# Performance work log

Measured on AMD Instinct MI355X. Metric: run time of the kernel, lower is better.

Reference implementation:

```python
import jax, jax.numpy as jnp
import numpy as np

# ---- static config (mirrors Net.__init__) ----
N_NODES, N_EDGES = 4000, 20000
N_PROTS, D = 919, 512            # node_emb: Embedding(919, 512); F_in = D (divide_input=False)
TOWERS, F_OUT = 4, D // 4        # F_out = out_channels // towers = 128
EDGE_D = 50
N_GRAPHS, N_CLASSES = 32, 10
N_LAYERS = 2
EPS_BN, EPS_STD = 1e-5, 1e-5

# deg histogram passed to PNAConv; only avg_deg['log'] matters for the scalers used
DEG_HIST = np.array([0., 800., 1200., 900., 600., 300., 150., 50.])
AVG_DEG_LOG = float((np.log(np.arange(DEG_HIST.size) + 1.0) * DEG_HIST).sum() / DEG_HIST.sum())


def setup_inputs() -> dict:
    key = jax.random.key(0)
    ks = jax.random.split(key, 16)
    g = lambda i, shape, s=0.05: (jax.random.normal(ks[i], shape, jnp.float32) * s)
    return dict(
        node_emb_w=g(0, (N_PROTS, D), 0.1),
        edge_emb_w=g(1, (2, EDGE_D), 0.1),
        pe_w=g(2, (2, D)), pe_b=jnp.zeros((D,), jnp.float32),
        edge_enc_w=g(3, (N_LAYERS, EDGE_D, D)), edge_enc_b=jnp.zeros((N_LAYERS, D), jnp.float32),
        pre_w=g(4, (N_LAYERS, TOWERS, 3 * D, D)), pre_b=jnp.zeros((N_LAYERS, TOWERS, D), jnp.float32),
        post_w=g(5, (N_LAYERS, TOWERS, 13 * D, F_OUT)), post_b=jnp.zeros((N_LAYERS, TOWERS, F_OUT), jnp.float32),
        lin_w=g(6, (N_LAYERS, D, D)), lin_b=jnp.zeros((N_LAYERS, D), jnp.float32),
        bn_gamma=jnp.ones((N_LAYERS, D), jnp.float32), bn_beta=jnp.zeros((N_LAYERS, D), jnp.float32),
        acts=jax.random.normal(ks[7], (N_NODES, 2), jnp.float32),
        fc1_w=g(8, (D, 2 * D)), fc1_b=jnp.zeros((2 * D,), jnp.float32),
        fc_out_w=g(9, (2 * D, N_CLASSES)), fc_out_b=jnp.zeros((N_CLASSES,), jnp.float32),
        prelu_a=jnp.float32(0.25),
        global_idx=jax.random.randint(ks[10], (N_NODES,), 0, N_PROTS),
        sign=jax.random.randint(ks[11], (N_EDGES,), 0, 2),
        edge_index=jax.random.randint(ks[12], (2, N_EDGES), 0, N_NODES),
        batch=jnp.sort(jax.random.randint(ks[13], (N_NODES,), 0, N_GRAPHS)),
    )


def _pna_layer(x, src, dst, e, pre_w, pre_b, post_w, post_b, lin_w, lin_b):
    # x: [N, D], e: [E, D] (edge_encoder output), pre_w: [T, 3D, D], post_w: [T, 13D, F_OUT]
    N, E = x.shape[0], src.shape[0]
    # pre-NN on cat([x_i, x_j, edge_attr]) expressed as split matmuls (pre_layers=1 -> single Linear)
    Wi, Wj, We = pre_w[:, :D], pre_w[:, D:2 * D], pre_w[:, 2 * D:]
    m = (jnp.einsum('ef,tfd->etd', x[dst], Wi)
         + jnp.einsum('ef,tfd->etd', x[src], Wj)
         + jnp.einsum('ef,tfd->etd', e, We) + pre_b)          # [E, T, D]
    # multi-aggregation at destination nodes: mean / min / max / std
    cnt = jax.ops.segment_sum(jnp.ones((E,), m.dtype), dst, N)  # in-degree
    has = (cnt > 0)[:, None, None]
    deg = jnp.maximum(cnt, 1.0)[:, None, None]                  # clamp(1) as in PyG
    s1 = jax.ops.segment_sum(m, dst, N)
    s2 = jax.ops.segment_sum(m * m, dst, N)
    mean = s1 / deg
    std = jnp.sqrt(jax.nn.relu(s2 / deg - mean * mean) + EPS_STD)
    mn = jnp.where(has, jax.ops.segment_min(m, dst, N), 0.0)
    mx = jnp.where(has, jax.ops.segment_max(m, dst, N), 0.0)
    agg = jnp.concatenate([mean, mn, mx, std], axis=-1)         # [N, T, 4D]
    # degree scalers: identity, amplification, attenuation
    amp = jnp.log(deg + 1.0) / AVG_DEG_LOG
    out = jnp.concatenate([agg, agg * amp, agg / amp], axis=-1)  # [N, T, 12D]
    # post-NN on cat([x, out]) as split matmuls (post_layers=1)
    Wx, Wo = post_w[:, :D], post_w[:, D:]
    o = (jnp.einsum('nf,tfd->ntd', x, Wx)
         + jnp.einsum('ntf,tfd->ntd', out, Wo) + post_b)        # [N, T, F_OUT]
    return o.reshape(N, TOWERS * F_OUT) @ lin_w + lin_b         # [N, D]


def reference(node_emb_w, edge_emb_w, pe_w, pe_b, edge_enc_w, edge_enc_b,
              pre_w, pre_b, post_w, post_b, lin_w, lin_b, bn_gamma, bn_beta,
              acts, fc1_w, fc1_b, fc_out_w, fc_out_b, prelu_a,
              global_idx, sign, edge_index, batch):
    src, dst = edge_index[0], edge_index[1]
    x = node_emb_w[global_idx] + (acts @ pe_w + pe_b)           # node_emb + PostEncoding
    ea = edge_emb_w[sign]                                       # [E, 50]
    for l in range(N_LAYERS):
        e = ea @ edge_enc_w[l] + edge_enc_b[l]                  # shared edge encoder
        h = _pna_layer(x, src, dst, e, pre_w[l], pre_b[l], post_w[l], post_b[l], lin_w[l], lin_b[l])
        mu = h.mean(axis=0)
        var = ((h - mu) ** 2).mean(axis=0)                      # training-mode BatchNorm (biased var)
        x = jax.nn.relu(bn_gamma[l] * (h - mu) * jax.lax.rsqrt(var + EPS_BN) + bn_beta[l])
    pooled = jax.ops.segment_sum(x, batch, N_GRAPHS)            # global_add_pool
    z = pooled @ fc1_w + fc1_b
    z = jnp.where(z > 0, z, prelu_a * z)                        # PReLU
    logits = z @ fc_out_w + fc_out_b
    return jax.nn.log_softmax(logits, axis=-1)
```

## Files before the change

### kernel.cpp

```cpp
#include <hip/hip_runtime.h>
#include <hip/hip_bf16.h>
#include <float.h>

#define NN 4000
#define NE 20000
#define DD 512
#define NT 4
#define FO 128
#define NG 32
#define NC 10
#define XGW 4096
#define AVGLOG 1.2548916493836102f
#define EPS_STD_ 1e-5f
#define EPS_BN_ 1e-5f

typedef __bf16 bf16x8 __attribute__((ext_vector_type(8)));
typedef float  f32x4  __attribute__((ext_vector_type(4)));

__device__ __forceinline__ void async_copy16(const void* g, void* l) {
    __builtin_amdgcn_global_load_lds((const __attribute__((address_space(1))) void*)g,
                                     (__attribute__((address_space(3))) void*)l, 16, 0, 0);
}

__global__ __launch_bounds__(256) void k_xg(const __bf16* __restrict__ XB, const __bf16* __restrict__ WCAT,
                                            const float* __restrict__ pb,
                                            __bf16* __restrict__ XG, float* __restrict__ OF,
                                            float* __restrict__ BN, float* __restrict__ PL, int zero_pl) {
    const int m0 = blockIdx.y * 128, n0 = blockIdx.x * 128;
    __shared__ __bf16 As[2 * 128 * 32];
    __shared__ __bf16 Bs[2 * 128 * 32];
    const int tid = threadIdx.x;
    const int wave = tid >> 6, lane = tid & 63;
    const int wm = (wave >> 1) * 64, wn = (wave & 1) * 64;
    const int fr = lane & 15, fq = lane >> 4;
    const int fk = fq * 8;
    const int srow = lane >> 2, skc = (lane & 3) * 8;

    f32x4 acc[4][4];
    const f32x4 zero = {0.f, 0.f, 0.f, 0.f};
#pragma unroll
    for (int i = 0; i < 4; ++i)
#pragma unroll
        for (int j = 0; j < 4; ++j) acc[i][j] = zero;

    for (int k0 = 0; k0 < 512; k0 += 64) {
#pragma unroll
        for (int p = 0; p < 2; ++p) {
#pragma unroll
            for (int q = 0; q < 2; ++q) {
                const int row = wave * 32 + q * 16 + srow;
                int ar = m0 + row; if (ar > NN - 1) ar = NN - 1;
                async_copy16(XB + (size_t)ar * 512 + k0 + p * 32 + skc,
                             As + p * 4096 + wave * 1024 + q * 512);
                async_copy16(WCAT + (size_t)(n0 + row) * 512 + k0 + p * 32 + skc,
                             Bs + p * 4096 + wave * 1024 + q * 512);
            }
        }
        __syncthreads();
#pragma unroll
        for (int p = 0; p < 2; ++p) {
            bf16x8 af[4], bfr[4];
#pragma unroll
            for (int mi = 0; mi < 4; ++mi) af[mi]  = *(const bf16x8*)(As + p * 4096 + (wm + mi * 16 + fr) * 32 + fk);
#pragma unroll
            for (int ni = 0; ni < 4; ++ni) bfr[ni] = *(const bf16x8*)(Bs + p * 4096 + (wn + ni * 16 + fr) * 32 + fk);
#pragma unroll
            for (int mi = 0; mi < 4; ++mi)
#pragma unroll
                for (int ni = 0; ni < 4; ++ni)
                    acc[mi][ni] = __builtin_amdgcn_mfma_f32_16x16x32_bf16(af[mi], bfr[ni], acc[mi][ni], 0, 0, 0);
        }
        __syncthreads();
    }
    if (n0 < 4096) {
#pragma unroll
        for (int mi = 0; mi < 4; ++mi) {
#pragma unroll
            for (int ni = 0; ni < 4; ++ni) {
                const int col = n0 + wn + ni * 16 + fr;
                const int rb = m0 + wm + mi * 16 + fq * 4;
#pragma unroll
                for (int r = 0; r < 4; ++r) {
                    const int rowc = rb + r;
                    if (rowc < NN) XG[(size_t)rowc * XGW + col] = (__bf16)acc[mi][ni][r];
                }
            }
        }
    } else {
        const int ocb = n0 - 4096;
#pragma unroll
        for (int mi = 0; mi < 4; ++mi) {
#pragma unroll
            for (int ni = 0; ni < 4; ++ni) {
                const int oc = ocb + wn + ni * 16 + fr;
                const float bv = pb[oc];
                const int rb = m0 + wm + mi * 16 + fq * 4;
#pragma unroll
                for (int r = 0; r < 4; ++r) {
                    const int rowc = rb + r;
                    if (rowc < NN) OF[(size_t)rowc * 512 + oc] = acc[mi][ni][r] + bv;
                }
            }
        }
    }
    if (blockIdx.x == 32 && blockIdx.y == 0) {
        BN[tid] = 0.f; BN[256 + tid] = 0.f; BN[512 + tid] = 0.f; BN[768 + tid] = 0.f;
        if (zero_pl)
            for (int i = tid; i < NG * DD; i += 256) PL[i] = 0.f;
    }
}

__global__ __launch_bounds__(256) void k_gw(const __bf16* __restrict__ AB, const __bf16* __restrict__ WTT,
                                            const float* __restrict__ amp, const float* __restrict__ ramp,
                                            __bf16* __restrict__ GWPb) {
    const int t = blockIdx.z & 3, kh = blockIdx.z >> 2;
    const int xg = blockIdx.x;
    const int m0 = blockIdx.y * 128;
    const __bf16* A  = AB  + (size_t)t * 2048 + (size_t)kh * 1024;
    const __bf16* BT = WTT + (size_t)t * 384 * 2048 + (size_t)xg * 128 * 2048 + (size_t)kh * 1024;
    __shared__ __bf16 As[2 * 128 * 32];
    __shared__ __bf16 Bs[2 * 128 * 32];
    const int tid = threadIdx.x;
    const int wave = tid >> 6, lane = tid & 63;
    const int wm = (wave >> 1) * 64, wn = (wave & 1) * 64;
    const int fr = lane & 15, fq = lane >> 4;
    const int fk = fq * 8;
    const int srow = lane >> 2, skc = (lane & 3) * 8;

    f32x4 acc[4][4];
    const f32x4 zero = {0.f, 0.f, 0.f, 0.f};
#pragma unroll
    for (int i = 0; i < 4; ++i)
#pragma unroll
        for (int j = 0; j < 4; ++j) acc[i][j] = zero;

    for (int k0 = 0; k0 < 1024; k0 += 64) {
#pragma unroll
        for (int p = 0; p < 2; ++p) {
#pragma unroll
            for (int q = 0; q < 2; ++q) {
                const int row = wave * 32 + q * 16 + srow;
                int ar = m0 + row; if (ar > NN - 1) ar = NN - 1;
                async_copy16(A + (size_t)ar * 8192 + k0 + p * 32 + skc,
                             As + p * 4096 + wave * 1024 + q * 512);
                async_copy16(BT + (size_t)row * 2048 + k0 + p * 32 + skc,
                             Bs + p * 4096 + wave * 1024 + q * 512);
            }
        }
        __syncthreads();
#pragma unroll
        for (int p = 0; p < 2; ++p) {
            bf16x8 af[4], bfr[4];
#pragma unroll
            for (int mi = 0; mi < 4; ++mi) af[mi]  = *(const bf16x8*)(As + p * 4096 + (wm + mi * 16 + fr) * 32 + fk);
#pragma unroll
            for (int ni = 0; ni < 4; ++ni) bfr[ni] = *(const bf16x8*)(Bs + p * 4096 + (wn + ni * 16 + fr) * 32 + fk);
#pragma unroll
            for (int mi = 0; mi < 4; ++mi)
#pragma unroll
                for (int ni = 0; ni < 4; ++ni)
                    acc[mi][ni] = __builtin_amdgcn_mfma_f32_16x16x32_bf16(af[mi], bfr[ni], acc[mi][ni], 0, 0, 0);
        }
        __syncthreads();
    }
    const int p = xg * 2 + kh;
    __bf16* P = GWPb + (size_t)p * NN * 512 + (size_t)t * 128;
#pragma unroll
    for (int mi = 0; mi < 4; ++mi) {
        const int rb = m0 + wm + mi * 16 + fq * 4;
#pragma unroll
        for (int r = 0; r < 4; ++r) {
            const int row = rb + r;
            if (row < NN) {
                const float w = (xg == 0) ? 1.0f : (xg == 1 ? amp[row] : ramp[row]);
#pragma unroll
                for (int ni = 0; ni < 4; ++ni)
                    P[(size_t)row * 512 + wn + ni * 16 + fr] = (__bf16)(acc[mi][ni][r] * w);
            }
        }
    }
}

__global__ void k_combine(const float* __restrict__ OF, const __bf16* __restrict__ GWPb,
                          __bf16* __restrict__ OB) {
    const size_t idx8 = ((size_t)blockIdx.x * 256 + threadIdx.x) * 8;
    float4 o0 = *(const float4*)(OF + idx8);
    float4 o1 = *(const float4*)(OF + idx8 + 4);
    float s[8] = {o0.x, o0.y, o0.z, o0.w, o1.x, o1.y, o1.z, o1.w};
#pragma unroll
    for (int p = 0; p < 6; ++p) {
        bf16x8 g = *(const bf16x8*)(GWPb + (size_t)p * NN * 512 + idx8);
#pragma unroll
        for (int i = 0; i < 8; ++i) s[i] += (float)g[i];
    }
    bf16x8 ov;
#pragma unroll
    for (int i = 0; i < 8; ++i) ov[i] = (__bf16)s[i];
    *(bf16x8*)(OB + idx8) = ov;
}

__global__ __launch_bounds__(256) void k_lin(const __bf16* __restrict__ OB, const __bf16* __restrict__ WLINT,
                                             const float* __restrict__ bl, float* __restrict__ H,
                                             float* __restrict__ BN) {
    const int n0c = blockIdx.x * 128, m0 = blockIdx.y * 64;
    __shared__ __bf16 As[64 * 32];
    __shared__ __bf16 Bs[128 * 32];
    __shared__ float bnS[128], bnQ[128];
    const int tid = threadIdx.x;
    if (tid < 128) { bnS[tid] = 0.f; bnQ[tid] = 0.f; }
    const int wave = tid >> 6, lane = tid & 63;
    const int wr = wave >> 1, wc = wave & 1;
    const int fr = lane & 15, fq = lane >> 4;
    f32x4 acc[2][4];
    const f32x4 zero = {0.f, 0.f, 0.f, 0.f};
#pragma unroll
    for (int i = 0; i < 2; ++i)
#pragma unroll
        for (int j = 0; j < 4; ++j) acc[i][j] = zero;

    const int ar = tid >> 2, akc = (tid & 3) * 8;
    int arow = m0 + ar; if (arow > NN - 1) arow = NN - 1;
    for (int k0 = 0; k0 < 512; k0 += 32) {
        async_copy16(OB + (size_t)arow * 512 + k0 + akc, As + tid * 8);
#pragma unroll
        for (int i = 0; i < 2; ++i) {
            const int cb = tid + 256 * i;
            const int br = cb >> 2, bkc = (cb & 3) * 8;
            async_copy16(WLINT + (size_t)(n0c + br) * 512 + k0 + bkc, Bs + cb * 8);
        }
        __syncthreads();
        bf16x8 a[2], b[4];
#pragma unroll
        for (int mi = 0; mi < 2; ++mi) a[mi] = *(const bf16x8*)(As + (wr * 32 + mi * 16 + fr) * 32 + fq * 8);
#pragma unroll
        for (int ni = 0; ni < 4; ++ni) b[ni] = *(const bf16x8*)(Bs + (wc * 64 + ni * 16 + fr) * 32 + fq * 8);
#pragma unroll
        for (int mi = 0; mi < 2; ++mi)
#pragma unroll
            for (int ni = 0; ni < 4; ++ni)
                acc[mi][ni] = __builtin_amdgcn_mfma_f32_16x16x32_bf16(a[mi], b[ni], acc[mi][ni], 0, 0, 0);
        __syncthreads();
    }
#pragma unroll
    for (int ni = 0; ni < 4; ++ni) {
        const int lc = wc * 64 + ni * 16 + fr;
        const int col = n0c + lc;
        const float bv = bl[col];
        float s = 0.f, q = 0.f;
#pragma unroll
        for (int mi = 0; mi < 2; ++mi) {
#pragma unroll
            for (int r = 0; r < 4; ++r) {
                const int rowc = m0 + wr * 32 + mi * 16 + fq * 4 + r;
                if (rowc < NN) {
                    const float v = acc[mi][ni][r] + bv;
                    H[(size_t)rowc * 512 + col] = v;
                    s += v; q += v * v;
                }
            }
        }
        atomicAdd(&bnS[lc], s); atomicAdd(&bnQ[lc], q);
    }
    __syncthreads();
    if (tid < 128) {
        atomicAdd(&BN[n0c + tid], bnS[tid]);
        atomicAdd(&BN[512 + n0c + tid], bnQ[tid]);
    }
}

__device__ __forceinline__ void tr32(const float* __restrict__ S, int sld,
                                     __bf16* __restrict__ D, int dld, int tx, int ty) {
    __shared__ float t[32][33];
    const int y0 = ty * 4;
#pragma unroll
    for (int i = 0; i < 4; ++i) t[y0 + i][tx] = S[(size_t)(y0 + i) * sld + tx];
    __syncthreads();
#pragma unroll
    for (int i = 0; i < 4; ++i) D[(size_t)(y0 + i) * dld + tx] = (__bf16)t[tx][y0 + i];
}

__global__ __launch_bounds__(256) void k_tr(const float* __restrict__ pre_w, const float* __restrict__ post_w,
                                            const float* __restrict__ lin_w,
                                            const float* __restrict__ eemb, const float* __restrict__ eew_b,
                                            const float* __restrict__ eeb_b, const float* __restrict__ pre_b,
                                            __bf16* __restrict__ WCAT, __bf16* __restrict__ WTT,
                                            __bf16* __restrict__ WLINT, float* __restrict__ EM) {
    int id = blockIdx.x;
    const int lay = (id >= 5696) ? 1 : 0;
    id -= lay * 5696;
    const float* pw   = pre_w  + (size_t)lay * NT * 3 * 512 * 512;
    const float* pow_ = post_w + (size_t)lay * NT * 6656 * 128;
    const float* lw   = lin_w  + (size_t)lay * 512 * 512;
    const float* eew  = eew_b  + (size_t)lay * 50 * 512;
    const float* eeb  = eeb_b  + (size_t)lay * 512;
    const float* pb   = pre_b  + (size_t)lay * NT * 512;
    __bf16* WCATl  = WCAT  + (size_t)lay * 4608 * 512;
    __bf16* WTTl   = WTT   + (size_t)lay * NT * 384 * 2048;
    __bf16* WLINTl = WLINT + (size_t)lay * 512 * 512;
    float*  EMl    = EM    + (size_t)lay * 4096;
    const int tx = threadIdx.x & 31, ty = threadIdx.x >> 5;
    if (id < 2048) {
        const int z = id >> 8, r = id & 255;
        const int t = z & 3, half = z >> 2;
        const int x = r & 15, y = r >> 4;
        const float* S = pw + ((size_t)(t * 1536 + half * 512 + y * 32)) * 512 + x * 32;
        __bf16* D = WCATl + ((size_t)(half * 2048 + t * 512 + x * 32)) * 512 + y * 32;
        tr32(S, 512, D, 512, tx, ty);
    } else if (id < 2304) {
        const int id3 = id - 2048;
        const int t = id3 >> 6, r = id3 & 63;
        const int x = r & 3, y = r >> 2;
        const float* S = pow_ + ((size_t)(t * 6656 + y * 32)) * 128 + x * 32;
        __bf16* D = WCATl + ((size_t)(4096 + t * 128 + x * 32)) * 512 + y * 32;
        tr32(S, 128, D, 512, tx, ty);
    } else if (id < 5376) {
        const int id4 = id - 2304;
        const int z = id4 >> 8, r = id4 & 255;
        const int t = z / 3, w = z % 3;
        const int x = r & 3, y = r >> 2;
        const float* S = pow_ + ((size_t)(t * 6656 + 512 + w * 2048 + y * 32)) * 128 + x * 32;
        __bf16* D = WTTl + (size_t)t * 384 * 2048 + ((size_t)(w * 128 + x * 32)) * 2048 + y * 32;
        tr32(S, 128, D, 2048, tx, ty);
    } else if (id < 5632) {
        const int r = id - 5376;
        const int x = r & 15, y = r >> 4;
        const float* S = lw + (size_t)y * 32 * 512 + x * 32;
        __bf16* D = WLINTl + (size_t)x * 32 * 512 + y * 32;
        tr32(S, 512, D, 512, tx, ty);
    } else {
        __shared__ float eks[512];
        __shared__ float part[4][64];
        const int tid = threadIdx.x;
        const int id5 = id - 5632;
        const int k = id5 >> 5;
        const int g0 = (id5 & 31) * 64;
#pragma unroll
        for (int h = 0; h < 2; ++h) {
            const int f = tid + h * 256;
            float s = eeb[f];
            for (int c = 0; c < 50; ++c) s += eemb[k * 50 + c] * eew[(size_t)c * 512 + f];
            eks[f] = s;
        }
        __syncthreads();
        const int wave = tid >> 6, lane = tid & 63;
        const int g = g0 + lane;
        const int t = g >> 9, d = g & 511;
        const float* Wp = pw + ((size_t)(t * 1536 + 1024)) * 512 + d;
        float s = 0.f;
        const int f0 = wave * 128;
#pragma unroll 4
        for (int f = f0; f < f0 + 128; ++f) s += eks[f] * Wp[(size_t)f * 512];
        part[wave][lane] = s;
        __syncthreads();
        if (tid < 64) {
            const int gg = g0 + tid;
            EMl[k * 2048 + gg] = pb[gg] + part[0][tid] + part[1][tid] + part[2][tid] + part[3][tid];
        }
    }
}

__global__ void k_count(const int* __restrict__ dst, int* __restrict__ cnt) {
    int e = blockIdx.x * 256 + threadIdx.x;
    if (e < NE) atomicAdd(&cnt[dst[e]], 1);
}

__global__ __launch_bounds__(1024) void k_scan_bx(const int* __restrict__ cnt, int* __restrict__ offs,
                                                  float* __restrict__ amp, float* __restrict__ ramp,
                                                  const float* __restrict__ nemb, const float* __restrict__ acts,
                                                  const float* __restrict__ pew, const float* __restrict__ peb,
                                                  const int* __restrict__ gidx, __bf16* __restrict__ XB) {
    const int t = threadIdx.x;
    if (blockIdx.x == 0) {
        __shared__ int part[1024];
        const int base = t * 4;
        int loc[4]; int s = 0;
#pragma unroll
        for (int i = 0; i < 4; ++i) { int v = (base + i < NN) ? cnt[base + i] : 0; loc[i] = s; s += v; }
        part[t] = s;
        __syncthreads();
        for (int o = 1; o < 1024; o <<= 1) {
            int v = (t >= o) ? part[t - o] : 0;
            __syncthreads();
            part[t] += v;
            __syncthreads();
        }
        const int pre = (t > 0) ? part[t - 1] : 0;
#pragma unroll
        for (int i = 0; i < 4; ++i) if (base + i < NN) offs[base + i] = pre + loc[i];
        if (t == 1023) offs[NN] = part[1023];
        for (int n = t; n < NN; n += 1024) {
            float deg = fmaxf((float)cnt[n], 1.0f);
            float a = logf(deg + 1.0f) / AVGLOG;
            amp[n] = a; ramp[n] = 1.0f / a;
        }
    } else {
        const int idx = (blockIdx.x - 1) * 1024 + t;
        const int n = idx >> 9, d = idx & 511;
        float v = nemb[(size_t)gidx[n] * DD + d] + acts[n * 2] * pew[d] + acts[n * 2 + 1] * pew[DD + d] + peb[d];
        XB[idx] = (__bf16)v;
    }
}

__global__ void k_fill(const int* __restrict__ src, const int* __restrict__ dst,
                       const int* __restrict__ sgn, const int* __restrict__ offs,
                       int* __restrict__ fill, int* __restrict__ epack) {
    int e = blockIdx.x * 256 + threadIdx.x;
    if (e < NE) {
        int d = dst[e];
        int pos = offs[d] + atomicAdd(&fill[d], 1);
        epack[pos] = (src[e] << 1) | sgn[e];
    }
}

__global__ __launch_bounds__(256) void k_agg(const __bf16* __restrict__ XG, const float* __restrict__ EM,
                                             const int* __restrict__ offs, const int* __restrict__ cnt,
                                             const int* __restrict__ epack, __bf16* __restrict__ AB) {
    const int n = blockIdx.x;
    const int g = threadIdx.x * 8;
    __shared__ int se[64];
    const int j0 = offs[n];
    const int deg = offs[n + 1] - j0;
    const int degc = deg < 64 ? deg : 64;
    if (threadIdx.x < degc) se[threadIdx.x] = epack[j0 + threadIdx.x];
    __syncthreads();
    float xid[8], em0[8], em1[8];
    {
        bf16x8 xb = *(const bf16x8*)(XG + (size_t)n * XGW + g);
#pragma unroll
        for (int i = 0; i < 8; ++i) xid[i] = (float)xb[i];
    }
    *(float4*)&em0[0] = *(const float4*)&EM[g];
    *(float4*)&em0[4] = *(const float4*)&EM[g + 4];
    *(float4*)&em1[0] = *(const float4*)&EM[2048 + g];
    *(float4*)&em1[4] = *(const float4*)&EM[2048 + g + 4];
    float s1[8], s2[8], mn[8], mx[8];
#pragma unroll
    for (int i = 0; i < 8; ++i) { s1[i] = 0.f; s2[i] = 0.f; mn[i] = FLT_MAX; mx[i] = -FLT_MAX; }

    int jj = 0;
    for (; jj + 2 <= degc; jj += 2) {
        const int e0 = se[jj], e1 = se[jj + 1];
        bf16x8 x0 = *(const bf16x8*)(XG + (size_t)(e0 >> 1) * XGW + 2048 + g);
        bf16x8 x1 = *(const bf16x8*)(XG + (size_t)(e1 >> 1) * XGW + 2048 + g);
        const int sg0 = e0 & 1, sg1 = e1 & 1;
#pragma unroll
        for (int i = 0; i < 8; ++i) {
            float m = xid[i] + (float)x0[i] + (sg0 ? em1[i] : em0[i]);
            s1[i] += m; s2[i] += m * m;
            mn[i] = fminf(mn[i], m); mx[i] = fmaxf(mx[i], m);
        }
#pragma unroll
        for (int i = 0; i < 8; ++i) {
            float m = xid[i] + (float)x1[i] + (sg1 ? em1[i] : em0[i]);
            s1[i] += m; s2[i] += m * m;
            mn[i] = fminf(mn[i], m); mx[i] = fmaxf(mx[i], m);
        }
    }
    if (jj < degc) {
        const int e0 = se[jj];
        bf16x8 x0 = *(const bf16x8*)(XG + (size_t)(e0 >> 1) * XGW + 2048 + g);
        const int sg0 = e0 & 1;
#pragma unroll
        for (int i = 0; i < 8; ++i) {
            float m = xid[i] + (float)x0[i] + (sg0 ? em1[i] : em0[i]);
            s1[i] += m; s2[i] += m * m;
            mn[i] = fminf(mn[i], m); mx[i] = fmaxf(mx[i], m);
        }
    }
    for (int j = 64; j < deg; ++j) {
        const int e0 = epack[j0 + j];
        bf16x8 x0 = *(const bf16x8*)(XG + (size_t)(e0 >> 1) * XGW + 2048 + g);
        const int sg0 = e0 & 1;
#pragma unroll
        for (int i = 0; i < 8; ++i) {
            float m = xid[i] + (float)x0[i] + (sg0 ? em1[i] : em0[i]);
            s1[i] += m; s2[i] += m * m;
            mn[i] = fminf(mn[i], m); mx[i] = fmaxf(mx[i], m);
        }
    }
    const int c = deg;
    const float degf = fmaxf((float)c, 1.0f);
    const float rdeg = 1.0f / degf;
    bf16x8 vmean, vmn, vmx, vsd;
#pragma unroll
    for (int i = 0; i < 8; ++i) {
        float mean = s1[i] * rdeg;
        float var = s2[i] * rdeg - mean * mean;
        float sd = sqrtf(fmaxf(var, 0.f) + EPS_STD_);
        float mnv = (c == 0) ? 0.f : mn[i];
        float mxv = (c == 0) ? 0.f : mx[i];
        vmean[i] = (__bf16)mean; vmn[i] = (__bf16)mnv; vmx[i] = (__bf16)mxv; vsd[i] = (__bf16)sd;
    }
    const int t = g >> 9, d = g & 511;
    __bf16* base = AB + (size_t)n * 8192 + (size_t)t * 2048 + d;
    *(bf16x8*)(base + 0 * DD) = vmean;
    *(bf16x8*)(base + 1 * DD) = vmn;
    *(bf16x8*)(base + 2 * DD) = vmx;
    *(bf16x8*)(base + 3 * DD) = vsd;
}

__global__ void k_bnapply(const float* __restrict__ H, const float* __restrict__ BN,
                          const float* __restrict__ gamma, const float* __restrict__ beta,
                          __bf16* __restrict__ XB, float* __restrict__ PL,
                          const int* __restrict__ batch, int last) {
    int idx = blockIdx.x * 256 + threadIdx.x;
    int n = idx >> 9, d = idx & 511;
    float mu = BN[d] * (1.0f / NN);
    float var = BN[512 + d] * (1.0f / NN) - mu * mu;
    float v = gamma[d] * (H[idx] - mu) * rsqrtf(var + EPS_BN_) + beta[d];
    v = fmaxf(v, 0.f);
    if (last) atomicAdd(&PL[(size_t)batch[n] * DD + d], v);
    else XB[idx] = (__bf16)v;
}

__global__ __launch_bounds__(128) void k_fc1(const float* __restrict__ PL, const float* __restrict__ W1,
                                             const float* __restrict__ b1, const float* __restrict__ pa,
                                             float* __restrict__ Z) {
    const int g = blockIdx.x >> 3;
    const int j = (blockIdx.x & 7) * 128 + threadIdx.x;
    __shared__ float pl[512];
    for (int i = threadIdx.x; i < 512; i += 128) pl[i] = PL[(size_t)g * 512 + i];
    __syncthreads();
    const float* w = W1 + j;
    float s0 = 0.f, s1 = 0.f, s2 = 0.f, s3 = 0.f;
#pragma unroll 2
    for (int f = 0; f < 512; f += 4) {
        s0 += pl[f + 0] * w[(size_t)(f + 0) * 1024];
        s1 += pl[f + 1] * w[(size_t)(f + 1) * 1024];
        s2 += pl[f + 2] * w[(size_t)(f + 2) * 1024];
        s3 += pl[f + 3] * w[(size_t)(f + 3) * 1024];
    }
    float s = b1[j] + ((s0 + s1) + (s2 + s3));
    const float a = *pa;
    Z[(size_t)g * 1024 + j] = s > 0.f ? s : a * s;
}

__global__ __launch_bounds__(64) void k_out(const float* __restrict__ Z, const float* __restrict__ Wo,
                                            const float* __restrict__ bo, float* __restrict__ out) {
    const int g = blockIdx.x, t = threadIdx.x;
    float part[NC];
#pragma unroll
    for (int c = 0; c < NC; ++c) part[c] = 0.f;
    for (int f = t; f < 1024; f += 64) {
        const float zv = Z[(size_t)g * 1024 + f];
#pragma unroll
        for (int c = 0; c < NC; ++c) part[c] += zv * Wo[(size_t)f * NC + c];
    }
#pragma unroll
    for (int off = 32; off > 0; off >>= 1)
#pragma unroll
        for (int c = 0; c < NC; ++c) part[c] += __shfl_down(part[c], off);
    if (t == 0) {
        float lg[NC], mxv = -FLT_MAX;
#pragma unroll
        for (int c = 0; c < NC; ++c) { lg[c] = part[c] + bo[c]; mxv = fmaxf(mxv, lg[c]); }
        float se = 0.f;
#pragma unroll
        for (int c = 0; c < NC; ++c) se += expf(lg[c] - mxv);
        const float lse = mxv + logf(se);
#pragma unroll
        for (int c = 0; c < NC; ++c) out[g * NC + c] = lg[c] - lse;
    }
}

extern "C" void kernel_launch(void* const* d_in, const int* in_sizes, int n_in,
                              void* d_out, int out_size, void* d_ws, size_t ws_size,
                              hipStream_t stream) {
    const float* node_emb_w = (const float*)d_in[0];
    const float* edge_emb_w = (const float*)d_in[1];
    const float* pe_w   = (const float*)d_in[2];
    const float* pe_b   = (const float*)d_in[3];
    const float* edge_enc_w = (const float*)d_in[4];
    const float* edge_enc_b = (const float*)d_in[5];
    const float* pre_w  = (const float*)d_in[6];
    const float* pre_b  = (const float*)d_in[7];
    const float* post_w = (const float*)d_in[8];
    const float* post_b = (const float*)d_in[9];
    const float* lin_w  = (const float*)d_in[10];
    const float* lin_b  = (const float*)d_in[11];
    const float* bn_gamma = (const float*)d_in[12];
    const float* bn_beta  = (const float*)d_in[13];
    const float* acts   = (const float*)d_in[14];
    const float* fc1_w  = (const float*)d_in[15];
    const float* fc1_b  = (const float*)d_in[16];
    const float* fc_out_w = (const float*)d_in[17];
    const float* fc_out_b = (const float*)d_in[18];
    const float* prelu_a  = (const float*)d_in[19];
    const int* global_idx = (const int*)d_in[20];
    const int* sgn        = (const int*)d_in[21];
    const int* edge_index = (const int*)d_in[22];
    const int* batch      = (const int*)d_in[23];
    float* out = (float*)d_out;

    char* W = (char*)d_ws;
    size_t off = 0;
    auto alloc = [&](size_t bytes) { void* p = W + off; off += (bytes + 63) & ~(size_t)63; return p; };
    __bf16* XB    = (__bf16*)alloc((size_t)NN * DD * 2);
    float*  H     = (float*)alloc((size_t)NN * DD * 4);
    __bf16* XG    = (__bf16*)alloc((size_t)NN * XGW * 2);
    __bf16* AB    = (__bf16*)alloc((size_t)NN * 8192 * 2);
    float*  OF    = (float*)alloc((size_t)NN * DD * 4);
    __bf16* GWPb  = (__bf16*)alloc((size_t)6 * NN * 512 * 2);
    __bf16* OB    = (__bf16*)alloc((size_t)NN * DD * 2);
    __bf16* WCAT  = (__bf16*)alloc((size_t)2 * 4608 * 512 * 2);
    __bf16* WTT   = (__bf16*)alloc((size_t)2 * NT * 384 * 2048 * 2);
    __bf16* WLINT = (__bf16*)alloc((size_t)2 * 512 * 512 * 2);
    float*  EM    = (float*)alloc((size_t)2 * 2 * 2048 * 4);
    float*  BN    = (float*)alloc(1024 * 4);
    float*  PL    = (float*)alloc((size_t)NG * DD * 4);
    float*  ZB    = (float*)alloc((size_t)NG * 1024 * 4);
    float*  AMP   = (float*)alloc(NN * 4);
    float*  RAMP  = (float*)alloc(NN * 4);
    int*    CNT   = (int*)alloc(NN * 4);
    int*    FILL  = (int*)alloc(NN * 4);
    int*    OFFS  = (int*)alloc((NN + 1) * 4);
    int*    EPACK = (int*)alloc(NE * 4);

    const int* src = edge_index;
    const int* dst = edge_index + NE;

    hipMemsetAsync(CNT, 0, 2 * NN * sizeof(int), stream);
    k_count<<<(NE + 255) / 256, 256, 0, stream>>>(dst, CNT);
    k_scan_bx<<<2001, 1024, 0, stream>>>(CNT, OFFS, AMP, RAMP,
                                         node_emb_w, acts, pe_w, pe_b, global_idx, XB);
    k_fill<<<(NE + 255) / 256, 256, 0, stream>>>(src, dst, sgn, OFFS, FILL, EPACK);
    k_tr<<<2 * 5696, 256, 0, stream>>>(pre_w, post_w, lin_w,
                                       edge_emb_w, edge_enc_w, edge_enc_b, pre_b,
                                       WCAT, WTT, WLINT, EM);

    for (int l = 0; l < 2; ++l) {
        const float* post_b_l = post_b + (size_t)l * NT * FO;
        const float* lin_b_l  = lin_b  + (size_t)l * DD;
        __bf16* WCATl  = WCAT  + (size_t)l * 4608 * 512;
        __bf16* WTTl   = WTT   + (size_t)l * NT * 384 * 2048;
        __bf16* WLINTl = WLINT + (size_t)l * 512 * 512;
        float*  EMl    = EM    + (size_t)l * 4096;

        k_xg<<<dim3(36, 32), 256, 0, stream>>>(XB, WCATl, post_b_l, XG, OF, BN, PL, l == 1);
        k_agg<<<NN, 256, 0, stream>>>(XG, EMl, OFFS, CNT, EPACK, AB);
        k_gw<<<dim3(3, 32, 8), 256, 0, stream>>>(AB, WTTl, AMP, RAMP, GWPb);
        k_combine<<<NN * DD / 2048, 256, 0, stream>>>(OF, GWPb, OB);
        k_lin<<<dim3(4, 63), 256, 0, stream>>>(OB, WLINTl, lin_b_l, H, BN);
        k_bnapply<<<NN * DD / 256, 256, 0, stream>>>(H, BN, bn_gamma + (size_t)l * DD,
                                                     bn_beta + (size_t)l * DD, XB, PL, batch, l == 1);
    }

    k_fc1<<<256, 128, 0, stream>>>(PL, fc1_w, fc1_b, prelu_a, ZB);
    k_out<<<NG, 64, 0, stream>>>(ZB, fc_out_w, fc_out_b, out);
}
```

Measured before the change: 492.1 us.

## Remap k_gw grid for XCD-local A reuse and halve K-step LDS tile

Flattens the k_gw 3D grid into a 1D grid of 768 blocks, remapped so the three xg blocks sharing the same A tile land on the same XCD and can reuse it from that XCD's L2. It also shrinks the per-iteration K tile from 64 to 32, which halves LDS use per block and may raise occupancy. The cost is twice as many barriers and load rounds per K sweep, with less latency hidden per sync.

```diff
diff --git a/kernel.cpp b/kernel.cpp
--- a/kernel.cpp
+++ b/kernel.cpp
@@ -113,13 +113,19 @@
 __global__ __launch_bounds__(256) void k_gw(const __bf16* __restrict__ AB, const __bf16* __restrict__ WTT,
                                             const float* __restrict__ amp, const float* __restrict__ ramp,
                                             __bf16* __restrict__ GWPb) {
-    const int t = blockIdx.z & 3, kh = blockIdx.z >> 2;
-    const int xg = blockIdx.x;
-    const int m0 = blockIdx.y * 128;
+    const int bid = blockIdx.x;
+    const int xcd = bid & 7;
+    const int q = bid >> 3;
+    const int xg = q % 3;
+    const int ghi = q / 3;
+    const int g = ghi * 8 + xcd;
+    const int y = g & 31, z = g >> 5;
+    const int t = z & 3, kh = z >> 2;
+    const int m0 = y * 128;
     const __bf16* A  = AB  + (size_t)t * 2048 + (size_t)kh * 1024;
     const __bf16* BT = WTT + (size_t)t * 384 * 2048 + (size_t)xg * 128 * 2048 + (size_t)kh * 1024;
-    __shared__ __bf16 As[2 * 128 * 32];
-    __shared__ __bf16 Bs[2 * 128 * 32];
+    __shared__ __bf16 As[128 * 32];
+    __shared__ __bf16 Bs[128 * 32];
     const int tid = threadIdx.x;
     const int wave = tid >> 6, lane = tid & 63;
     const int wm = (wave >> 1) * 64, wn = (wave & 1) * 64;
@@ -134,33 +140,25 @@
 #pragma unroll
         for (int j = 0; j < 4; ++j) acc[i][j] = zero;
 
-    for (int k0 = 0; k0 < 1024; k0 += 64) {
+    for (int k0 = 0; k0 < 1024; k0 += 32) {
 #pragma unroll
         for (int p = 0; p < 2; ++p) {
-#pragma unroll
-            for (int q = 0; q < 2; ++q) {
-                const int row = wave * 32 + q * 16 + srow;
-                int ar = m0 + row; if (ar > NN - 1) ar = NN - 1;
-                async_copy16(A + (size_t)ar * 8192 + k0 + p * 32 + skc,
-                             As + p * 4096 + wave * 1024 + q * 512);
-                async_copy16(BT + (size_t)row * 2048 + k0 + p * 32 + skc,
-                             Bs + p * 4096 + wave * 1024 + q * 512);
-            }
-        }
-        __syncthreads();
-#pragma unroll
-        for (int p = 0; p < 2; ++p) {
-            bf16x8 af[4], bfr[4];
-#pragma unroll
-            for (int mi = 0; mi < 4; ++mi) af[mi]  = *(const bf16x8*)(As + p * 4096 + (wm + mi * 16 + fr) * 32 + fk);
-#pragma unroll
-            for (int ni = 0; ni < 4; ++ni) bfr[ni] = *(const bf16x8*)(Bs + p * 4096 + (wn + ni * 16 + fr) * 32 + fk);
-#pragma unroll
-            for (int mi = 0; mi < 4; ++mi)
-#pragma unroll
-                for (int ni = 0; ni < 4; ++ni)
-                    acc[mi][ni] = __builtin_amdgcn_mfma_f32_16x16x32_bf16(af[mi], bfr[ni], acc[mi][ni], 0, 0, 0);
-        }
+            const int row = wave * 32 + p * 16 + srow;
+            int ar = m0 + row; if (ar > NN - 1) ar = NN - 1;
+            async_copy16(A + (size_t)ar * 8192 + k0 + skc, As + wave * 1024 + p * 512);
+            async_copy16(BT + (size_t)row * 2048 + k0 + skc, Bs + wave * 1024 + p * 512);
+        }
+        __syncthreads();
+        bf16x8 af[4], bfr[4];
+#pragma unroll
+        for (int mi = 0; mi < 4; ++mi) af[mi]  = *(const bf16x8*)(As + (wm + mi * 16 + fr) * 32 + fk);
+#pragma unroll
+        for (int ni = 0; ni < 4; ++ni) bfr[ni] = *(const bf16x8*)(Bs + (wn + ni * 16 + fr) * 32 + fk);
+#pragma unroll
+        for (int mi = 0; mi < 4; ++mi)
+#pragma unroll
+            for (int ni = 0; ni < 4; ++ni)
+                acc[mi][ni] = __builtin_amdgcn_mfma_f32_16x16x32_bf16(af[mi], bfr[ni], acc[mi][ni], 0, 0, 0);
         __syncthreads();
     }
     const int p = xg * 2 + kh;
@@ -638,7 +636,7 @@
 
         k_xg<<<dim3(36, 32), 256, 0, stream>>>(XB, WCATl, post_b_l, XG, OF, BN, PL, l == 1);
         k_agg<<<NN, 256, 0, stream>>>(XG, EMl, OFFS, CNT, EPACK, AB);
-        k_gw<<<dim3(3, 32, 8), 256, 0, stream>>>(AB, WTTl, AMP, RAMP, GWPb);
+        k_gw<<<768, 256, 0, stream>>>(AB, WTTl, AMP, RAMP, GWPb);
         k_combine<<<NN * DD / 2048, 256, 0, stream>>>(OF, GWPb, OB);
         k_lin<<<dim3(4, 63), 256, 0, stream>>>(OB, WLINTl, lin_b_l, H, BN);
         k_bnapply<<<NN * DD / 256, 256, 0, stream>>>(H, BN, bn_gamma + (size_t)l * DD,
```

Measured after the change: 474.2 us. -3.6%, faster.
